# Performance work log

Measured on AMD Instinct MI355X. Metric: run time of the kernel, lower is better.

Reference implementation:

```python
import jax, jax.numpy as jnp
import numpy as np

WINDOW_SIZE = 11
SIGMA = 1.5
C1 = 0.01 ** 2
C2 = 0.03 ** 2


def _gaussian_window_3d(window_size=WINDOW_SIZE, sigma=SIGMA):
    # 1D gaussian, normalized, then separable outer product -> dense 3D kernel
    x = jnp.arange(window_size, dtype=jnp.float32)
    g = jnp.exp(-((x - window_size // 2) ** 2) / (2.0 * sigma ** 2))
    g = g / g.sum()
    w3 = g[:, None, None] * g[None, :, None] * g[None, None, :]  # [ws,ws,ws]
    return w3[None, None]  # [O=1, I=1, D, H, W]


def _conv3d_same(x, w):
    # x: [N,1,D,H,W], w: [1,1,ws,ws,ws]; 'SAME' padding matches torch padding=ws//2 for odd ws
    return jax.lax.conv_general_dilated(
        x, w, window_strides=(1, 1, 1), padding='SAME',
        dimension_numbers=('NCDHW', 'OIDHW', 'NCDHW'))


def setup_inputs() -> dict:
    key = jax.random.key(0)
    k1, k2 = jax.random.split(key)
    shape = (4, 1, 160, 160, 160)
    img1 = jax.random.uniform(k1, shape, dtype=jnp.float32)
    img2 = jax.random.uniform(k2, shape, dtype=jnp.float32)
    return {"img1": img1, "img2": img2}


def reference(img1, img2):
    window = _gaussian_window_3d()
    mu1 = _conv3d_same(img1, window)
    mu2 = _conv3d_same(img2, window)
    mu1_sq = mu1 * mu1
    mu2_sq = mu2 * mu2
    mu1_mu2 = mu1 * mu2
    sigma1_sq = _conv3d_same(img1 * img1, window) - mu1_sq
    sigma2_sq = _conv3d_same(img2 * img2, window) - mu2_sq
    sigma12 = _conv3d_same(img1 * img2, window) - mu1_mu2
    ssim_map = ((2.0 * mu1_mu2 + C1) * (2.0 * sigma12 + C2)) / (
        (mu1_sq + mu2_sq + C1) * (sigma1_sq + sigma2_sq + C2))
    return 1.0 - ssim_map.mean()
```

## Files before the change

### kernel.cpp

```cpp
#include <hip/hip_runtime.h>
#include <hip/hip_bf16.h>
#include <math.h>

#define WW     160
#define NBATCH 4
#define VOL    (160*160*160)
#define PLANE  (160*160)

#define C1f 0.0001f
#define C2f 0.0009f

#define RUN_H 16
#define NROWS (RUN_H + 10)
#define LDW   176
#define RUN_D 20
#define PF    5

typedef float v2f __attribute__((ext_vector_type(2)));

struct Gw { float g[11]; };

__device__ __forceinline__ float bf2f(unsigned short u) {
    return __uint_as_float(((unsigned int)u) << 16);
}
__device__ __forceinline__ unsigned short f2bf(float f) {
    __hip_bfloat16 h = __float2bfloat16(f);
    return *reinterpret_cast<unsigned short*>(&h);
}

__global__ __launch_bounds__(192, 5) void k_wh(
    const float* __restrict__ x, const float* __restrict__ y,
    ushort4* __restrict__ B4, unsigned short* __restrict__ B1, Gw gw)
{
    __shared__ unsigned int tile[NROWS][LDW];
    const int t  = threadIdx.x;
    const int h0 = blockIdx.x * RUN_H;
    const int d  = blockIdx.y;
    const int n  = blockIdx.z;

    const float* xb = x + (size_t)n * VOL + (size_t)d * PLANE;
    const float* yb = y + (size_t)n * VOL + (size_t)d * PLANE;

#pragma unroll 4
    for (int s = t; s < NROWS * LDW; s += 192) {
        int r = s / LDW, c = s - r * LDW;
        int h = h0 - 5 + r;
        int w = c - 5;
        float vx = 0.f, vy = 0.f;
        if (h >= 0 && h < 160 && w >= 0 && w < 160) {
            size_t idx = (size_t)h * WW + w;
            vx = xb[idx];
            vy = yb[idx];
        }
        tile[r][c] = ((unsigned int)f2bf(vy) << 16) | (unsigned int)f2bf(vx);
    }
    __syncthreads();

    if (t < 160) {
        const int w = t;
        const size_t outbase = (size_t)n * VOL + (size_t)d * PLANE + w;
        v2f ring01[11], ring23[11];
        float ring4[11];
#pragma unroll
        for (int i = 0; i < NROWS; ++i) {
            v2f a01 = {0.f, 0.f}, a23 = {0.f, 0.f};
            float a4 = 0.f;
#pragma unroll
            for (int k = 0; k < 5; ++k) {
                unsigned int u1 = tile[i][w + k];
                unsigned int u2 = tile[i][w + 10 - k];
                v2f xy1 = { __uint_as_float(u1 << 16), __uint_as_float(u1 & 0xffff0000u) };
                v2f xy2 = { __uint_as_float(u2 << 16), __uint_as_float(u2 & 0xffff0000u) };
                float g  = gw.g[k];
                v2f g2 = {g, g};
                a01 += g2 * (xy1 + xy2);
                v2f sq = xy1 * xy1;
                sq += xy2 * xy2;
                a23 += g2 * sq;
                float p = xy1.x * xy1.y;
                p = fmaf(xy2.x, xy2.y, p);
                a4 += g * p;
            }
            {
                unsigned int u = tile[i][w + 5];
                v2f xy = { __uint_as_float(u << 16), __uint_as_float(u & 0xffff0000u) };
                float g  = gw.g[5];
                v2f g2 = {g, g};
                a01 += g2 * xy;
                a23 += g2 * (xy * xy);
                a4  += g * (xy.x * xy.y);
            }
            ring01[i%11] = a01; ring23[i%11] = a23; ring4[i%11] = a4;

            if (i >= 10) {
                const int j = i - 10;
                v2f o01 = {0.f, 0.f}, o23 = {0.f, 0.f};
                float o4 = 0.f;
#pragma unroll
                for (int k = 0; k < 11; ++k) {
                    float g = gw.g[k];
                    v2f g2 = {g, g};
                    o01 += g2 * ring01[(j + k) % 11];
                    o23 += g2 * ring23[(j + k) % 11];
                    o4  += g  * ring4 [(j + k) % 11];
                }
                size_t oi = outbase + (size_t)(h0 + j) * WW;
                ushort4 u4;
                u4.x = f2bf(o01.x); u4.y = f2bf(o01.y);
                u4.z = f2bf(o23.x); u4.w = f2bf(o23.y);
                B4[oi] = u4;
                B1[oi] = f2bf(o4);
            }
        }
    }
}

__global__ __launch_bounds__(256, 4) void k_dssim(
    const ushort4* __restrict__ B4, const unsigned short* __restrict__ B1,
    double* __restrict__ accum, Gw gw)
{
    const int tid = threadIdx.x;
    const int p   = blockIdx.x * 256 + tid;
    const int d0  = blockIdx.y * RUN_D;
    const int n   = blockIdx.z;
    const size_t base = (size_t)n * VOL + p;

    v2f ring01[11], ring23[11];
    float ring4[11];
    float lsum = 0.f;

    ushort4 pf4[PF];
    unsigned short pf1[PF];
    {
        const bool front_ok = (d0 != 0);
#pragma unroll
        for (int q = 0; q < PF; ++q) {
            pf4[q] = make_ushort4(0,0,0,0);
            pf1[q] = 0;
            if (front_ok) {
                size_t idx = base + (size_t)(d0 - 5 + q) * PLANE;
                pf4[q] = B4[idx];
                pf1[q] = B1[idx];
            }
        }
    }

#pragma unroll
    for (int i = 0; i < RUN_D + 10; ++i) {
        ushort4 c4 = pf4[i % PF];
        unsigned short c1 = pf1[i % PF];
        ring01[i%11] = (v2f){ bf2f(c4.x), bf2f(c4.y) };
        ring23[i%11] = (v2f){ bf2f(c4.z), bf2f(c4.w) };
        ring4 [i%11] = bf2f(c1);

        if (i + PF < RUN_D + 10) {
            const int dd = d0 + i;
            bool ok = true;
            if (i >= RUN_D) ok = (d0 != 160 - RUN_D);
            pf4[i % PF] = make_ushort4(0,0,0,0);
            pf1[i % PF] = 0;
            if (ok) {
                size_t idx = base + (size_t)dd * PLANE;
                pf4[i % PF] = B4[idx];
                pf1[i % PF] = B1[idx];
            }
        }

        if (i >= 10) {
            const int j = i - 10;
            v2f o01 = {0.f, 0.f}, o23 = {0.f, 0.f};
            float o4 = 0.f;
#pragma unroll
            for (int k = 0; k < 11; ++k) {
                float g = gw.g[k];
                v2f g2 = {g, g};
                o01 += g2 * ring01[(j + k) % 11];
                o23 += g2 * ring23[(j + k) % 11];
                o4  += g  * ring4 [(j + k) % 11];
            }
            float mu1 = o01.x, mu2 = o01.y;
            float e11 = o23.x, e22 = o23.y, e12 = o4;
            float m11 = mu1 * mu2;
            float num = (2.f * m11 + C1f) * (2.f * (e12 - m11) + C2f);
            float den = (mu1 * mu1 + mu2 * mu2 + C1f) *
                        ((e11 - mu1 * mu1) + (e22 - mu2 * mu2) + C2f);
            lsum += num / den;
        }
    }

    __shared__ float wsum[4];
    const int lane = tid & 63, wi = tid >> 6;
#pragma unroll
    for (int off = 32; off > 0; off >>= 1)
        lsum += __shfl_down(lsum, off, 64);
    if (lane == 0) wsum[wi] = lsum;
    __syncthreads();
    if (tid == 0)
        atomicAdd(accum, (double)(wsum[0] + wsum[1] + wsum[2] + wsum[3]));
}

__global__ void k_final(const double* __restrict__ accum, float* __restrict__ out)
{
    out[0] = (float)(1.0 - accum[0] / ((double)NBATCH * (double)VOL));
}

extern "C" void kernel_launch(void* const* d_in, const int* in_sizes, int n_in,
                              void* d_out, int out_size, void* d_ws, size_t ws_size,
                              hipStream_t stream)
{
    const float* img1 = (const float*)d_in[0];
    const float* img2 = (const float*)d_in[1];
    float* out = (float*)d_out;

    char* ws = (char*)d_ws;
    ushort4* B4 = (ushort4*)ws;
    unsigned short* B1 = (unsigned short*)(ws + (size_t)NBATCH * VOL * 8);
    double* accum = (double*)(ws + (size_t)NBATCH * VOL * 10);

    Gw gw;
    {
        double gd[11], s = 0.0;
        for (int i = 0; i < 11; ++i) {
            double t = (double)(i - 5);
            gd[i] = exp(-(t * t) / (2.0 * 1.5 * 1.5));
            s += gd[i];
        }
        for (int i = 0; i < 11; ++i) gw.g[i] = (float)(gd[i] / s);
    }

    hipMemsetAsync(accum, 0, sizeof(double), stream);

    k_wh   <<<dim3(160 / RUN_H, 160, NBATCH), 192, 0, stream>>>(img1, img2, B4, B1, gw);
    k_dssim<<<dim3(PLANE / 256, 160 / RUN_D, NBATCH), 256, 0, stream>>>(B4, B1, accum, gw);
    k_final<<<1, 1, 0, stream>>>(accum, out);
}
```

Measured before the change: 305.8 us.

## Pack sum of squares into one channel to drop separate B1 intermediate buffer

SSIM only needs sigma1_sq + sigma2_sq, so the W/H pass now stores the sum of the two squared-image blurs in one bf16 lane and puts the cross term in the fourth lane. This removes the separate 2-byte B1 buffer, saving one write stream and one read stream, and cuts one ring of registers and FMAs in the depth pass. The depth kernel also deepens prefetch from 5 to 8, lowers the launch-bounds occupancy hint from 4 to 3, and uses a hardware reciprocal instead of a divide. The risks are extra bf16 rounding on the summed term, a less accurate reciprocal, and register pressure from the deeper prefetch.

```diff
diff --git a/kernel.cpp b/kernel.cpp
--- a/kernel.cpp
+++ b/kernel.cpp
@@ -14,7 +14,8 @@
 #define NROWS (RUN_H + 10)
 #define LDW   176
 #define RUN_D 20
-#define PF    5
+#define ITERS (RUN_D + 10)
+#define PF    8
 
 typedef float v2f __attribute__((ext_vector_type(2)));
 
@@ -30,7 +31,7 @@
 
 __global__ __launch_bounds__(192, 5) void k_wh(
     const float* __restrict__ x, const float* __restrict__ y,
-    ushort4* __restrict__ B4, unsigned short* __restrict__ B1, Gw gw)
+    ushort4* __restrict__ B4, Gw gw)
 {
     __shared__ unsigned int tile[NROWS][LDW];
     const int t  = threadIdx.x;
@@ -106,18 +107,18 @@
                 }
                 size_t oi = outbase + (size_t)(h0 + j) * WW;
                 ushort4 u4;
-                u4.x = f2bf(o01.x); u4.y = f2bf(o01.y);
-                u4.z = f2bf(o23.x); u4.w = f2bf(o23.y);
+                u4.x = f2bf(o01.x);
+                u4.y = f2bf(o01.y);
+                u4.z = f2bf(o23.x + o23.y);
+                u4.w = f2bf(o4);
                 B4[oi] = u4;
-                B1[oi] = f2bf(o4);
-            }
-        }
-    }
-}
-
-__global__ __launch_bounds__(256, 4) void k_dssim(
-    const ushort4* __restrict__ B4, const unsigned short* __restrict__ B1,
-    double* __restrict__ accum, Gw gw)
+            }
+        }
+    }
+}
+
+__global__ __launch_bounds__(256, 3) void k_dssim(
+    const ushort4* __restrict__ B4, double* __restrict__ accum, Gw gw)
 {
     const int tid = threadIdx.x;
     const int p   = blockIdx.x * 256 + tid;
@@ -126,65 +127,55 @@
     const size_t base = (size_t)n * VOL + p;
 
     v2f ring01[11], ring23[11];
-    float ring4[11];
     float lsum = 0.f;
 
-    ushort4 pf4[PF];
-    unsigned short pf1[PF];
+    ushort4 pf[PF];
     {
         const bool front_ok = (d0 != 0);
 #pragma unroll
         for (int q = 0; q < PF; ++q) {
-            pf4[q] = make_ushort4(0,0,0,0);
-            pf1[q] = 0;
-            if (front_ok) {
+            bool ok = (q >= 5) || front_ok;
+            pf[q] = make_ushort4(0, 0, 0, 0);
+            if (ok) {
                 size_t idx = base + (size_t)(d0 - 5 + q) * PLANE;
-                pf4[q] = B4[idx];
-                pf1[q] = B1[idx];
-            }
-        }
-    }
-
-#pragma unroll
-    for (int i = 0; i < RUN_D + 10; ++i) {
-        ushort4 c4 = pf4[i % PF];
-        unsigned short c1 = pf1[i % PF];
+                pf[q] = B4[idx];
+            }
+        }
+    }
+
+#pragma unroll
+    for (int i = 0; i < ITERS; ++i) {
+        ushort4 c4 = pf[i % PF];
         ring01[i%11] = (v2f){ bf2f(c4.x), bf2f(c4.y) };
         ring23[i%11] = (v2f){ bf2f(c4.z), bf2f(c4.w) };
-        ring4 [i%11] = bf2f(c1);
-
-        if (i + PF < RUN_D + 10) {
-            const int dd = d0 + i;
-            bool ok = true;
-            if (i >= RUN_D) ok = (d0 != 160 - RUN_D);
-            pf4[i % PF] = make_ushort4(0,0,0,0);
-            pf1[i % PF] = 0;
+
+        if (i + PF < ITERS) {
+            const int dd = d0 + i + 3;
+            const bool ok = (dd < 160);
+            pf[i % PF] = make_ushort4(0, 0, 0, 0);
             if (ok) {
                 size_t idx = base + (size_t)dd * PLANE;
-                pf4[i % PF] = B4[idx];
-                pf1[i % PF] = B1[idx];
+                pf[i % PF] = B4[idx];
             }
         }
 
         if (i >= 10) {
             const int j = i - 10;
             v2f o01 = {0.f, 0.f}, o23 = {0.f, 0.f};
-            float o4 = 0.f;
 #pragma unroll
             for (int k = 0; k < 11; ++k) {
                 float g = gw.g[k];
                 v2f g2 = {g, g};
                 o01 += g2 * ring01[(j + k) % 11];
                 o23 += g2 * ring23[(j + k) % 11];
-                o4  += g  * ring4 [(j + k) % 11];
             }
             float mu1 = o01.x, mu2 = o01.y;
-            float e11 = o23.x, e22 = o23.y, e12 = o4;
-            float m11 = mu1 * mu2;
+            float s   = o23.x, e12 = o23.y;
+            float m11  = mu1 * mu2;
+            float musq = fmaf(mu1, mu1, mu2 * mu2);
             float num = (2.f * m11 + C1f) * (2.f * (e12 - m11) + C2f);
-            float den = (mu1 * mu1 + mu2 * mu2 + C1f) *
-                        ((e11 - mu1 * mu1) + (e22 - mu2 * mu2) + C2f);
-            lsum += num / den;
+            float den = (musq + C1f) * ((s - musq) + C2f);
+            lsum += num * __builtin_amdgcn_rcpf(den);
         }
     }
 
@@ -214,8 +205,7 @@
 
     char* ws = (char*)d_ws;
     ushort4* B4 = (ushort4*)ws;
-    unsigned short* B1 = (unsigned short*)(ws + (size_t)NBATCH * VOL * 8);
-    double* accum = (double*)(ws + (size_t)NBATCH * VOL * 10);
+    double* accum = (double*)(ws + (size_t)NBATCH * VOL * 8);
 
     Gw gw;
     {
@@ -230,7 +220,7 @@
 
     hipMemsetAsync(accum, 0, sizeof(double), stream);
 
-    k_wh   <<<dim3(160 / RUN_H, 160, NBATCH), 192, 0, stream>>>(img1, img2, B4, B1, gw);
-    k_dssim<<<dim3(PLANE / 256, 160 / RUN_D, NBATCH), 256, 0, stream>>>(B4, B1, accum, gw);
+    k_wh   <<<dim3(160 / RUN_H, 160, NBATCH), 192, 0, stream>>>(img1, img2, B4, gw);
+    k_dssim<<<dim3(PLANE / 256, 160 / RUN_D, NBATCH), 256, 0, stream>>>(B4, accum, gw);
     k_final<<<1, 1, 0, stream>>>(accum, out);
 }
```

Result: faster. 297.6 us (-2.7%).
